# Kernel tuning notes

Hardware: AMD Instinct MI355X
Metric: run time of the kernel (lower is better)

## Reference

```python
import jax, jax.numpy as jnp
import numpy as np

DT = 0.5
TAU = 10.0
ALPHA = DT / TAU
GAMMA_MULT = 1.0


def setup_inputs() -> dict:
    key = jax.random.key(0)
    k1, k2, k3 = jax.random.split(key, 3)
    T, B, IN, N = 512, 128, 64, 1024
    H = 2 * N
    x = jax.random.normal(k1, (T, B, IN), dtype=jnp.float32)
    hidden0 = jax.random.uniform(k2, (B, H), dtype=jnp.float32)
    # wAttractor: fixed [H, H] ring-attractor weight matrix (generate_alpha_matrix stand-in)
    w_attractor = 0.01 * jax.random.normal(k3, (H, H), dtype=jnp.float32)
    # input_to_vel: Linear(IN, 1, bias=False), initialized to ones (trainable)
    w_in = jnp.ones((1, IN), dtype=jnp.float32)
    return {"x": x, "hidden0": hidden0, "w_attractor": w_attractor, "w_in": w_in}


def reference(x, hidden0, w_attractor, w_in):
    H = w_attractor.shape[0]
    n = H // 2
    # vel_to_ring frozen params: weight = gamma (shape [H,1]), bias = ones
    gamma = GAMMA_MULT * jnp.concatenate([-jnp.ones(n, x.dtype), jnp.ones(n, x.dtype)])
    # i2h for all timesteps at once: vel = x @ w_in.T -> [T,B,1]; i2h = vel*gamma + 1
    vel = jnp.einsum('tbi,oi->tbo', x, w_in)          # [T, B, 1]
    i2h = vel * gamma[None, None, :] + 1.0            # [T, B, H]

    def step(h, i2h_t):
        h2h = h @ w_attractor                          # [B, H]
        h_new = (1.0 - ALPHA) * h + ALPHA * jax.nn.relu(i2h_t + h2h)
        return h_new, h_new

    hT, acts = jax.lax.scan(step, hidden0, i2h)        # acts: [T, B, H]
    return acts, hT
```

## Files before the change

kernel.cpp:

```cpp
#include <hip/hip_runtime.h>

#define H_DIM   2048
#define N_HALF  1024
#define B_SZ    128
#define T_STEPS 512
#define IN_DIM  64
#define ALPHA_F 0.05f
#define OMA_F   0.95f

typedef __bf16 bf16x8 __attribute__((ext_vector_type(8)));
typedef float  f32x4  __attribute__((ext_vector_type(4)));
typedef unsigned int u32x4 __attribute__((ext_vector_type(4)));

__device__ __forceinline__ unsigned short f2bf(float f) {
    union { float f; unsigned int u; } v; v.f = f;
    unsigned int u = v.u;
    u += 0x7FFFu + ((u >> 16) & 1u);
    return (unsigned short)(u >> 16);
}

__device__ __forceinline__ unsigned long long ldA8(const unsigned long long* p) {
    return __hip_atomic_load(p, __ATOMIC_RELAXED, __HIP_MEMORY_SCOPE_AGENT);
}

__device__ __forceinline__ void pollflag(const unsigned* f, unsigned need, int lane) {
    if (lane == 0) {
        while (__hip_atomic_load(f, __ATOMIC_RELAXED, __HIP_MEMORY_SCOPE_AGENT) < need)
            __builtin_amdgcn_s_sleep(1);
    }
    asm volatile("" ::: "memory");
}

__global__ void wf_kernel(const float* __restrict__ W, unsigned short* __restrict__ Wf) {
    __shared__ float tile[64][65];
    const int jb = blockIdx.x * 64;
    const int kb = blockIdx.y * 64;
    const int t  = threadIdx.y * 64 + threadIdx.x;
    const int tx = threadIdx.x, ty = threadIdx.y;
    #pragma unroll
    for (int r = ty; r < 64; r += 4)
        tile[r][tx] = W[(size_t)(kb + r) * H_DIM + jb + tx];
    __syncthreads();
    #pragma unroll
    for (int cc = 0; cc < 2; ++cc) {
        const int c  = t * 2 + cc;
        const int jj = c >> 3;
        const int kc = c & 7;
        const int j  = jb + jj;
        const int k0 = kb + kc * 8;
        unsigned short v[8];
        #pragma unroll
        for (int e = 0; e < 8; ++e)
            v[e] = f2bf(tile[kc * 8 + e][jj]);
        const int ks = k0 >> 5;
        const int q4 = (k0 >> 3) & 3;
        const size_t dst = (size_t)(j >> 6) * 131072 +
                           ((size_t)(ks * 4 + q4) * 64 + (j & 63)) * 8;
        *reinterpret_cast<u32x4*>(Wf + dst) = *reinterpret_cast<u32x4*>(v);
    }
}

__global__ void vel_kernel(const float* __restrict__ x, const float* __restrict__ w_in,
                           float* __restrict__ vel) {
    const int tb = blockIdx.x * blockDim.x + threadIdx.x;
    if (tb >= T_STEPS * B_SZ) return;
    const float* xp = x + (size_t)tb * IN_DIM;
    float s = 0.f;
    #pragma unroll
    for (int i = 0; i < IN_DIM; i += 4) {
        float4 xv = *reinterpret_cast<const float4*>(xp + i);
        float4 wv = *reinterpret_cast<const float4*>(w_in + i);
        s += xv.x * wv.x + xv.y * wv.y + xv.z * wv.z + xv.w * wv.w;
    }
    vel[tb] = s;
}

__global__ void hbf_init_kernel(const float* __restrict__ h0, unsigned short* __restrict__ hbf) {
    const int i = blockIdx.x * blockDim.x + threadIdx.x;
    hbf[i] = f2bf(h0[i]);
}

__global__ __launch_bounds__(512, 1) void ring_coop_kernel(
        const unsigned short* __restrict__ Wf,
        unsigned short* __restrict__ hbf0,
        unsigned short* __restrict__ hbf1,
        const float* __restrict__ vel,
        const float* __restrict__ hidden0,
        float* __restrict__ acts,
        float* __restrict__ outT,
        unsigned* __restrict__ flags) {
    __shared__ __align__(16) unsigned char A_lds[65536];
    __shared__ __align__(16) f32x4 pacc[256];
    __shared__ __align__(16) float hbuf[16][64];

    const int tid = threadIdx.x;
    const int bid = blockIdx.x;
    const int colg = (bid & 7) * 4 + ((bid >> 3) & 3);
    const int rowg = bid >> 5;
    const int colbase = colg * 64;
    const int rowbase = rowg * 16;

    const int lane = tid & 63, w = tid >> 6;
    const int colq = w & 3, khalf = w >> 2;
    const int r16 = lane & 15, q4 = lane >> 4;
    const int j = colbase + colq * 16 + r16;
    const float gamma = (j < N_HALF) ? -1.0f : 1.0f;

    const int srow = lane >> 3;
    const int kcl  = lane & 7;

    unsigned* rflags = flags + rowg * 128;

    const unsigned short* bgbase = Wf + (size_t)colg * 131072
                                   + (size_t)(khalf * 128 + q4) * 512
                                   + (size_t)(colq * 16 + r16) * 8;
    bf16x8 Breg[32];
    #pragma unroll
    for (int s = 0; s < 32; ++s)
        Breg[s] = *reinterpret_cast<const bf16x8*>(bgbase + (size_t)s * 2048);

    f32x4 hreg = {0.f, 0.f, 0.f, 0.f};
    if (khalf == 0) {
        #pragma unroll
        for (int i = 0; i < 4; ++i)
            hreg[i] = hidden0[(size_t)(rowbase + q4 * 4 + i) * H_DIM + j];
    }

    const int xe = r16 ^ q4;
    const int xo = xe ^ 4;

    for (int t = 0; t < T_STEPS; ++t) {
        const unsigned short* hin  = (t & 1) ? hbf1 : hbf0;
        unsigned short*       hout = (t & 1) ? hbf0 : hbf1;
        const float* vel_t = vel + (size_t)t * B_SZ;
        float* acts_t = acts + (size_t)t * B_SZ * H_DIM;

        {
            int cg = (colg + 1 + w) & 31;
            pollflag(rflags + cg * 4, (unsigned)t, lane);
            const unsigned long long* ap = reinterpret_cast<const unsigned long long*>(
                hin + (size_t)(rowbase + srow) * H_DIM + cg * 64 + kcl * 8);
            unsigned long long p0 = ldA8(ap), p1 = ldA8(ap + 1);
            unsigned long long p2 = ldA8(ap + 4096), p3 = ldA8(ap + 4097);
            #pragma unroll
            for (int i = 0; i < 4; ++i) {
                unsigned long long n0 = 0, n1 = 0, n2 = 0, n3 = 0;
                int cgn = 0;
                if (i < 3) {
                    cgn = (colg + 1 + w + 8 * (i + 1)) & 31;
                    pollflag(rflags + cgn * 4, (unsigned)t, lane);
                    const unsigned long long* apn = reinterpret_cast<const unsigned long long*>(
                        hin + (size_t)(rowbase + srow) * H_DIM + cgn * 64 + kcl * 8);
                    n0 = ldA8(apn); n1 = ldA8(apn + 1);
                    n2 = ldA8(apn + 4096); n3 = ldA8(apn + 4097);
                }
                union { unsigned long long u[2]; u32x4 v; } lo, hi;
                lo.u[0] = p0; lo.u[1] = p1; hi.u[0] = p2; hi.u[1] = p3;
                *reinterpret_cast<u32x4*>(A_lds +
                    (size_t)((cg * 8 + kcl) * 16 + (srow ^ kcl)) * 16) = lo.v;
                *reinterpret_cast<u32x4*>(A_lds +
                    (size_t)((cg * 8 + kcl) * 16 + ((srow + 8) ^ kcl)) * 16) = hi.v;
                if (i < 3) { p0 = n0; p1 = n1; p2 = n2; p3 = n3; cg = cgn; }
            }
        }
        __syncthreads();

        const unsigned char* Abase = A_lds + (size_t)(khalf * 2048 + q4 * 16) * 16;
        f32x4 acc0 = {0.f,0.f,0.f,0.f}, acc1 = {0.f,0.f,0.f,0.f};
        f32x4 acc2 = {0.f,0.f,0.f,0.f}, acc3 = {0.f,0.f,0.f,0.f};
        #pragma unroll
        for (int s = 0; s < 32; s += 4) {
            bf16x8 a0 = *reinterpret_cast<const bf16x8*>(Abase +
                (size_t)((s + 0) * 64 + xe) * 16);
            bf16x8 a1 = *reinterpret_cast<const bf16x8*>(Abase +
                (size_t)((s + 1) * 64 + xo) * 16);
            bf16x8 a2 = *reinterpret_cast<const bf16x8*>(Abase +
                (size_t)((s + 2) * 64 + xe) * 16);
            bf16x8 a3 = *reinterpret_cast<const bf16x8*>(Abase +
                (size_t)((s + 3) * 64 + xo) * 16);
            acc0 = __builtin_amdgcn_mfma_f32_16x16x32_bf16(a0, Breg[s + 0], acc0, 0, 0, 0);
            acc1 = __builtin_amdgcn_mfma_f32_16x16x32_bf16(a1, Breg[s + 1], acc1, 0, 0, 0);
            acc2 = __builtin_amdgcn_mfma_f32_16x16x32_bf16(a2, Breg[s + 2], acc2, 0, 0, 0);
            acc3 = __builtin_amdgcn_mfma_f32_16x16x32_bf16(a3, Breg[s + 3], acc3, 0, 0, 0);
        }
        f32x4 psum = (acc0 + acc1) + (acc2 + acc3);

        if (khalf == 1) pacc[colq * 64 + lane] = psum;
        __syncthreads();
        if (khalf == 0) {
            const f32x4 h2h = psum + pacc[colq * 64 + lane];
            const f32x4 vel4 = *reinterpret_cast<const f32x4*>(vel_t + rowbase + q4 * 4);
            #pragma unroll
            for (int i = 0; i < 4; ++i) {
                const float pre = fmaf(vel4[i], gamma, 1.0f) + h2h[i];
                const float hn = OMA_F * hreg[i] + ALPHA_F * fmaxf(pre, 0.0f);
                hreg[i] = hn;
                hbuf[q4 * 4 + i][colq * 16 + r16] = hn;
            }
        }
        __syncthreads();

        if (tid < 256) {
            const int row3 = tid >> 4, c4 = (tid & 15) * 4;
            f32x4 va = *reinterpret_cast<const f32x4*>(&hbuf[row3][c4]);
            float* dst = acts_t + (size_t)(rowbase + row3) * H_DIM + colbase + c4;
            asm volatile("global_store_dwordx4 %0, %1, off sc0 sc1 nt"
                         :: "v"(dst), "v"(va) : "memory");
        } else if (tid < 384) {
            const int t2 = tid - 256;
            const int row2 = t2 >> 3, c8 = (t2 & 7) * 8;
            unsigned pk[4];
            #pragma unroll
            for (int e = 0; e < 4; ++e)
                pk[e] = (unsigned)f2bf(hbuf[row2][c8 + 2 * e]) |
                        ((unsigned)f2bf(hbuf[row2][c8 + 2 * e + 1]) << 16);
            u32x4 hv = {pk[0], pk[1], pk[2], pk[3]};
            unsigned short* dst = hout + (size_t)(rowbase + row2) * H_DIM + colbase + c8;
            asm volatile("global_store_dwordx4 %0, %1, off sc0 sc1"
                         :: "v"(dst), "v"(hv) : "memory");
            asm volatile("s_waitcnt vmcnt(0)" ::: "memory");
        } else if (t == T_STEPS - 1) {
            #pragma unroll
            for (int e = 0; e < 2; ++e) {
                const int idx = (tid - 384) * 2 + e;
                const int row3 = idx >> 4, c4 = (idx & 15) * 4;
                f32x4 va = *reinterpret_cast<const f32x4*>(&hbuf[row3][c4]);
                *reinterpret_cast<f32x4*>(outT +
                    (size_t)(rowbase + row3) * H_DIM + colbase + c4) = va;
            }
        }
        __syncthreads();
        if (tid == 0 && t < T_STEPS - 1)
            __hip_atomic_store(rflags + colg * 4, (unsigned)(t + 1),
                               __ATOMIC_RELAXED, __HIP_MEMORY_SCOPE_AGENT);
    }
}

__global__ __launch_bounds__(256) void step_kernel(
        const unsigned short* __restrict__ Wf,
        const unsigned short* __restrict__ hbf_in,
        unsigned short* __restrict__ hbf_out,
        const float* __restrict__ vel_t,
        const float* __restrict__ hprev,
        float* __restrict__ acts_t,
        float* __restrict__ outT) {
    const int lane = threadIdx.x & 63;
    const int w    = threadIdx.x >> 6;
    const int bid  = blockIdx.x;
    const int mg   = bid >> 7;
    const int n    = bid & 127;
    const int base_b = mg * 64 + w * 16;
    const int base_j = n * 16;
    const int r16  = lane & 15;
    const int q4   = lane >> 4;

    const int j = base_j + r16;
    const bf16x8* Ap = reinterpret_cast<const bf16x8*>(
        hbf_in + (size_t)(base_b + r16) * H_DIM + q4 * 8);
    const unsigned short* wslot = Wf + (size_t)(j >> 6) * 131072 + (size_t)(j & 63) * 8;

    f32x4 acc0 = {0.f, 0.f, 0.f, 0.f};
    f32x4 acc1 = {0.f, 0.f, 0.f, 0.f};
    #pragma unroll 8
    for (int kk = 0; kk < 32; ++kk) {
        bf16x8 a0 = Ap[kk * 4];
        bf16x8 a1 = Ap[kk * 4 + 128];
        bf16x8 b0 = *reinterpret_cast<const bf16x8*>(wslot + (size_t)(kk * 4 + q4) * 512);
        bf16x8 b1 = *reinterpret_cast<const bf16x8*>(wslot + (size_t)((kk + 32) * 4 + q4) * 512);
        acc0 = __builtin_amdgcn_mfma_f32_16x16x32_bf16(a0, b0, acc0, 0, 0, 0);
        acc1 = __builtin_amdgcn_mfma_f32_16x16x32_bf16(a1, b1, acc1, 0, 0, 0);
    }
    f32x4 h2h = acc0 + acc1;

    const float gamma = (j < N_HALF) ? -1.0f : 1.0f;
    const int brow0 = base_b + q4 * 4;
    #pragma unroll
    for (int i = 0; i < 4; ++i) {
        const int b = brow0 + i;
        const float v  = vel_t[b];
        const float hp = hprev[(size_t)b * H_DIM + j];
        const float pre = fmaf(v, gamma, 1.0f) + h2h[i];
        const float hn = OMA_F * hp + ALPHA_F * fmaxf(pre, 0.0f);
        acts_t[(size_t)b * H_DIM + j] = hn;
        hbf_out[(size_t)b * H_DIM + j] = f2bf(hn);
        if (outT) outT[(size_t)b * H_DIM + j] = hn;
    }
}

extern "C" void kernel_launch(void* const* d_in, const int* in_sizes, int n_in,
                              void* d_out, int out_size, void* d_ws, size_t ws_size,
                              hipStream_t stream) {
    const float* x       = (const float*)d_in[0];
    const float* hidden0 = (const float*)d_in[1];
    const float* w_attr  = (const float*)d_in[2];
    const float* w_in    = (const float*)d_in[3];

    float* acts = (float*)d_out;
    float* outT = acts + (size_t)T_STEPS * B_SZ * H_DIM;

    unsigned char* ws = (unsigned char*)d_ws;
    unsigned short* Wf   = (unsigned short*)ws;
    unsigned short* hbf0 = (unsigned short*)(ws + ((size_t)8 << 20));
    unsigned short* hbf1 = hbf0 + (size_t)B_SZ * H_DIM;
    float* vel = (float*)(ws + ((size_t)8 << 20) + (size_t)2 * B_SZ * H_DIM * 2);
    unsigned* flags = (unsigned*)(ws + ((size_t)8 << 20) + ((size_t)1 << 20) + (256 << 10));

    hipMemsetAsync(flags, 0, 4096, stream);
    wf_kernel<<<dim3(32, 32), dim3(64, 4), 0, stream>>>(w_attr, Wf);
    vel_kernel<<<(T_STEPS * B_SZ + 255) / 256, 256, 0, stream>>>(x, w_in, vel);
    hbf_init_kernel<<<(B_SZ * H_DIM + 255) / 256, 256, 0, stream>>>(hidden0, hbf0);

    void* args[] = {(void*)&Wf, (void*)&hbf0, (void*)&hbf1, (void*)&vel,
                    (void*)&hidden0, (void*)&acts, (void*)&outT, (void*)&flags};
    hipError_t rc = hipLaunchCooperativeKernel(
        reinterpret_cast<void*>(ring_coop_kernel),
        dim3(256), dim3(512), args, 0, stream);

    if (rc != hipSuccess) {
        for (int t = 0; t < T_STEPS; ++t) {
            const unsigned short* hin = (t & 1) ? hbf1 : hbf0;
            unsigned short* hout      = (t & 1) ? hbf0 : hbf1;
            const float* hprev = (t == 0) ? hidden0 : acts + (size_t)(t - 1) * B_SZ * H_DIM;
            step_kernel<<<256, 256, 0, stream>>>(
                Wf, hin, hout, vel + (size_t)t * B_SZ, hprev,
                acts + (size_t)t * B_SZ * H_DIM,
                (t == T_STEPS - 1) ? outT : nullptr);
        }
    }
}
```

Baseline: 2.180 ms.

## Replace per-column-group flag polling with single-wave bulk wait and plain loads

Measured after the change: 2.709 ms. 1.24x slower.

```diff
diff --git a/kernel.cpp b/kernel.cpp
--- a/kernel.cpp
+++ b/kernel.cpp
@@ -17,18 +17,6 @@
     unsigned int u = v.u;
     u += 0x7FFFu + ((u >> 16) & 1u);
     return (unsigned short)(u >> 16);
-}
-
-__device__ __forceinline__ unsigned long long ldA8(const unsigned long long* p) {
-    return __hip_atomic_load(p, __ATOMIC_RELAXED, __HIP_MEMORY_SCOPE_AGENT);
-}
-
-__device__ __forceinline__ void pollflag(const unsigned* f, unsigned need, int lane) {
-    if (lane == 0) {
-        while (__hip_atomic_load(f, __ATOMIC_RELAXED, __HIP_MEMORY_SCOPE_AGENT) < need)
-            __builtin_amdgcn_s_sleep(1);
-    }
-    asm volatile("" ::: "memory");
 }
 
 __global__ void wf_kernel(const float* __restrict__ W, unsigned short* __restrict__ Wf) {
@@ -95,8 +83,8 @@
 
     const int tid = threadIdx.x;
     const int bid = blockIdx.x;
-    const int colg = (bid & 7) * 4 + ((bid >> 3) & 3);
-    const int rowg = bid >> 5;
+    const int rowg = bid & 7;
+    const int colg = bid >> 3;
     const int colbase = colg * 64;
     const int rowbase = rowg * 16;
 
@@ -135,32 +123,33 @@
         const float* vel_t = vel + (size_t)t * B_SZ;
         float* acts_t = acts + (size_t)t * B_SZ * H_DIM;
 
+        if (w == 0) {
+            for (;;) {
+                int ok = 1;
+                if (lane < 32) {
+                    unsigned v = __hip_atomic_load(rflags + lane * 4,
+                                     __ATOMIC_RELAXED, __HIP_MEMORY_SCOPE_AGENT);
+                    ok = (v >= (unsigned)t);
+                }
+                if (__all(ok)) break;
+                __builtin_amdgcn_s_sleep(1);
+            }
+            asm volatile("buffer_inv sc1\n\ts_waitcnt vmcnt(0)" ::: "memory");
+        }
+        __syncthreads();
+
         {
-            int cg = (colg + 1 + w) & 31;
-            pollflag(rflags + cg * 4, (unsigned)t, lane);
-            const unsigned long long* ap = reinterpret_cast<const unsigned long long*>(
-                hin + (size_t)(rowbase + srow) * H_DIM + cg * 64 + kcl * 8);
-            unsigned long long p0 = ldA8(ap), p1 = ldA8(ap + 1);
-            unsigned long long p2 = ldA8(ap + 4096), p3 = ldA8(ap + 4097);
             #pragma unroll
             for (int i = 0; i < 4; ++i) {
-                unsigned long long n0 = 0, n1 = 0, n2 = 0, n3 = 0;
-                int cgn = 0;
-                if (i < 3) {
-                    cgn = (colg + 1 + w + 8 * (i + 1)) & 31;
-                    pollflag(rflags + cgn * 4, (unsigned)t, lane);
-                    const unsigned long long* apn = reinterpret_cast<const unsigned long long*>(
-                        hin + (size_t)(rowbase + srow) * H_DIM + cgn * 64 + kcl * 8);
-                    n0 = ldA8(apn); n1 = ldA8(apn + 1);
-                    n2 = ldA8(apn + 4096); n3 = ldA8(apn + 4097);
-                }
-                union { unsigned long long u[2]; u32x4 v; } lo, hi;
-                lo.u[0] = p0; lo.u[1] = p1; hi.u[0] = p2; hi.u[1] = p3;
+                const int cg = w * 4 + i;
+                const unsigned short* ap =
+                    hin + (size_t)(rowbase + srow) * H_DIM + cg * 64 + kcl * 8;
+                u32x4 lo = *reinterpret_cast<const u32x4*>(ap);
+                u32x4 hi = *reinterpret_cast<const u32x4*>(ap + 8 * H_DIM);
                 *reinterpret_cast<u32x4*>(A_lds +
-                    (size_t)((cg * 8 + kcl) * 16 + (srow ^ kcl)) * 16) = lo.v;
+                    (size_t)((cg * 8 + kcl) * 16 + (srow ^ kcl)) * 16) = lo;
                 *reinterpret_cast<u32x4*>(A_lds +
-                    (size_t)((cg * 8 + kcl) * 16 + ((srow + 8) ^ kcl)) * 16) = hi.v;
-                if (i < 3) { p0 = n0; p1 = n1; p2 = n2; p3 = n3; cg = cgn; }
+                    (size_t)((cg * 8 + kcl) * 16 + ((srow + 8) ^ kcl)) * 16) = hi;
             }
         }
         __syncthreads();
```
